# Kernel tuning notes

Measured on AMD Instinct MI355X. Metric: run time of the kernel, lower is better.

## Reference

```python
import jax, jax.numpy as jnp
import numpy as np

D = 1024
H = 16
HD = D // H
B = 2
T = 2048


def setup_inputs() -> dict:
    key = jax.random.key(0)
    ks = jax.random.split(key, 5)
    x = jax.random.normal(ks[0], (B, T, D), dtype=jnp.float32)
    # PyTorch SDPA bool-mask semantics: True = attend. Causal lower-triangular.
    attn_mask = jnp.tril(jnp.ones((T, T), dtype=bool))
    w_qkv = jax.random.normal(ks[1], (3 * D, D), dtype=jnp.float32) * (1.0 / np.sqrt(D))
    b_qkv = jax.random.normal(ks[2], (3 * D,), dtype=jnp.float32) * 0.02
    w_proj = jax.random.normal(ks[3], (D, D), dtype=jnp.float32) * (1.0 / np.sqrt(D))
    b_proj = jax.random.normal(ks[4], (D,), dtype=jnp.float32) * 0.02
    return {"x": x, "attn_mask": attn_mask, "w_qkv": w_qkv, "b_qkv": b_qkv,
            "w_proj": w_proj, "b_proj": b_proj}


def reference(x, attn_mask, w_qkv, b_qkv, w_proj, b_proj):
    b, t, d = x.shape
    # fused QKV projection (torch Linear: y = x @ W.T + b)
    qkv = jnp.einsum('btd,ed->bte', x, w_qkv) + b_qkv  # [B,T,3D]
    q, k, v = jnp.split(qkv, 3, axis=-1)
    # [B,T,D] -> [B,H,T,hd]
    def heads(z):
        return z.reshape(b, t, H, HD).transpose(0, 2, 1, 3)
    q, k, v = heads(q), heads(k), heads(v)
    scale = 1.0 / jnp.sqrt(jnp.asarray(HD, dtype=x.dtype))
    scores = jnp.einsum('bhqd,bhkd->bhqk', q, k) * scale  # [B,H,T,T]
    neg_inf = jnp.asarray(jnp.finfo(x.dtype).min, dtype=x.dtype)
    scores = jnp.where(attn_mask, scores, neg_inf)
    attn = jax.nn.softmax(scores, axis=-1)
    y = jnp.einsum('bhqk,bhkd->bhqd', attn, v)  # [B,H,T,hd]
    y = y.transpose(0, 2, 1, 3).reshape(b, t, d)
    y = jnp.einsum('btd,ed->bte', y, w_proj) + b_proj
    return y
```

## Files before the change

### kernel.cpp

```cpp
#include <hip/hip_runtime.h>
#include <hip/hip_bf16.h>
#include <math.h>

#define D_MODEL 1024
#define NHEAD   16
#define HDIM    64
#define BATCH   2
#define SEQ     2048
#define MTOT    (BATCH * SEQ)

typedef unsigned short u16;
typedef short short8 __attribute__((ext_vector_type(8)));
typedef short short4v __attribute__((ext_vector_type(4)));
typedef float floatx4 __attribute__((ext_vector_type(4)));

#define LOG2E 1.44269504088896340736f

static __device__ __forceinline__ u16 f2b(float f) {
  union { __hip_bfloat16 h; u16 u; } cv;
  cv.h = __float2bfloat16(f);
  return cv.u;
}

typedef const __attribute__((address_space(1))) unsigned int guint;
typedef __attribute__((address_space(3))) unsigned int luint;
static __device__ __forceinline__ void gl_lds16(const u16* g, u16* l) {
  __builtin_amdgcn_global_load_lds((guint*)g, (luint*)l, 16, 0, 0);
}

__global__ __launch_bounds__(256) void cast3_f2b(
    const float* __restrict__ a, u16* __restrict__ ao, int na,
    const float* __restrict__ b, u16* __restrict__ bo, int nb,
    const float* __restrict__ c, u16* __restrict__ co) {
  int i = (blockIdx.x * 256 + threadIdx.x) * 4;
  const float* src;
  u16* dst;
  if (i < na) {
    src = a + i;
    dst = ao + i;
  } else if (i < na + nb) {
    src = b + (i - na);
    dst = bo + (i - na);
  } else {
    src = c + (i - na - nb);
    dst = co + (i - na - nb);
  }
  float4 v = *(const float4*)src;
  ushort4 o;
  o.x = f2b(v.x);
  o.y = f2b(v.y);
  o.z = f2b(v.z);
  o.w = f2b(v.w);
  *(ushort4*)dst = o;
}

template <int MODE>
__global__ __launch_bounds__(256) void gemm_bt_bf16(
    const u16* __restrict__ A, const u16* __restrict__ Bm,
    const float* __restrict__ bias, u16* __restrict__ Cq, u16* __restrict__ Ck,
    u16* __restrict__ Cvt, float* __restrict__ Cf, int M, int N, int K) {
  __shared__ u16 smem[17408];
  u16(*As)[128][32] = (u16(*)[128][32])smem;
  u16(*Bs)[128][32] = (u16(*)[128][32])(smem + 8192);

  const int tid = threadIdx.x;
  const int lane = tid & 63;
  const int wave = tid >> 6;
  const int wm = (wave >> 1) * 64;
  const int wn = (wave & 1) * 64;
  const int quad = lane >> 4;
  const int l15 = lane & 15;
  const int m0 = blockIdx.y * 128;
  const int n0 = blockIdx.x * 128;

  const int srow = wave * 16 + (lane >> 2);
  const int k8 = (lane & 3) * 8;

  const u16* gA0 = A + (size_t)(m0 + srow) * K + k8;
  const u16* gA1 = A + (size_t)(m0 + srow + 64) * K + k8;
  const u16* gB0 = Bm + (size_t)(n0 + srow) * K + k8;
  const u16* gB1 = Bm + (size_t)(n0 + srow + 64) * K + k8;

  floatx4 acc[4][4];
#pragma unroll
  for (int i = 0; i < 4; ++i)
#pragma unroll
    for (int j = 0; j < 4; ++j)
#pragma unroll
      for (int e = 0; e < 4; ++e) acc[i][j][e] = 0.0f;

  gl_lds16(gA0, &As[0][srow][k8]);
  gl_lds16(gA1, &As[0][srow + 64][k8]);
  gl_lds16(gB0, &Bs[0][srow][k8]);
  gl_lds16(gB1, &Bs[0][srow + 64][k8]);

  const int niter = K / 32;
  for (int kt = 0; kt < niter; ++kt) {
    const int cur = kt & 1;
    __syncthreads();
    if (kt + 1 < niter) {
      const int k0n = (kt + 1) * 32;
      gl_lds16(gA0 + k0n, &As[cur ^ 1][srow][k8]);
      gl_lds16(gA1 + k0n, &As[cur ^ 1][srow + 64][k8]);
      gl_lds16(gB0 + k0n, &Bs[cur ^ 1][srow][k8]);
      gl_lds16(gB1 + k0n, &Bs[cur ^ 1][srow + 64][k8]);
    }
    short8 af[4], bf[4];
#pragma unroll
    for (int i = 0; i < 4; ++i)
      af[i] = *(const short8*)&As[cur][wm + i * 16 + l15][quad * 8];
#pragma unroll
    for (int j = 0; j < 4; ++j)
      bf[j] = *(const short8*)&Bs[cur][wn + j * 16 + l15][quad * 8];
#pragma unroll
    for (int i = 0; i < 4; ++i)
#pragma unroll
      for (int j = 0; j < 4; ++j)
        acc[i][j] = __builtin_amdgcn_mfma_f32_16x16x32_bf16(af[i], bf[j],
                                                            acc[i][j], 0, 0, 0);
  }

  if (MODE == 0) {
    const int nbase = n0 + wn;
    const int sel = nbase >> 10;
    const int h = (nbase >> 6) & (NHEAD - 1);
    if (sel == 2) {
#pragma unroll
      for (int j = 0; j < 4; ++j) {
        const int n = nbase + j * 16 + l15;
        const float bv = bias[n];
        const int d = n & (HDIM - 1);
#pragma unroll
        for (int i = 0; i < 4; ++i) {
          const int mb = m0 + wm + i * 16 + quad * 4;
          const int b = mb >> 11;
          const int t = mb & (SEQ - 1);
          ushort4 o4;
          o4.x = f2b(acc[i][j][0] + bv);
          o4.y = f2b(acc[i][j][1] + bv);
          o4.z = f2b(acc[i][j][2] + bv);
          o4.w = f2b(acc[i][j][3] + bv);
          *(ushort4*)(Cvt + ((size_t)(b * NHEAD + h) * HDIM + d) * SEQ + t) = o4;
        }
      }
    } else {
      u16* dst = (sel == 0) ? Cq : Ck;
      __syncthreads();
      u16(*Ct)[68] = (u16(*)[68])(smem + wave * 4352);
#pragma unroll
      for (int j = 0; j < 4; ++j) {
        const float bv = bias[nbase + j * 16 + l15];
#pragma unroll
        for (int i = 0; i < 4; ++i)
#pragma unroll
          for (int r = 0; r < 4; ++r)
            Ct[i * 16 + quad * 4 + r][j * 16 + l15] = f2b(acc[i][j][r] + bv);
      }
      const int mb0 = m0 + wm;
      const int b = mb0 >> 11;
      const int t0 = mb0 & (SEQ - 1);
      u16* rowbase = dst + ((size_t)(b * NHEAD + h) * SEQ + t0) * HDIM;
      const int tr = lane >> 3;
      const int d8 = (lane & 7) * 8;
#pragma unroll
      for (int p = 0; p < 8; ++p) {
        const int row = p * 8 + tr;
        *(short8*)(rowbase + (size_t)row * HDIM + d8) =
            *(const short8*)&Ct[row][d8];
      }
    }
  } else {
#pragma unroll
    for (int j = 0; j < 4; ++j) {
      const int n = n0 + wn + j * 16 + l15;
      const float bv = bias[n];
#pragma unroll
      for (int i = 0; i < 4; ++i) {
        const int mb = m0 + wm + i * 16 + quad * 4;
#pragma unroll
        for (int r = 0; r < 4; ++r)
          Cf[(size_t)(mb + r) * N + n] = acc[i][j][r] + bv;
      }
    }
  }
}

__global__ __launch_bounds__(512) void flash_mfma(const u16* __restrict__ Qg,
                                                  const u16* __restrict__ Kg,
                                                  const u16* __restrict__ Vtg,
                                                  u16* __restrict__ Yb) {
  __shared__ u16 Qs[128][72];
  __shared__ u16 Ks[64][72];
  __shared__ u16 Vt[80][72];
  __shared__ u16 Pb[128][76];

  const int tid = threadIdx.x;
  const int lane = tid & 63;
  const int wave = tid >> 6;
  const int wrow = wave * 16;
  const int quad = lane >> 4;
  const int l15 = lane & 15;
  const int bh = blockIdx.y;
  const int b = bh >> 4;
  const int h = bh & (NHEAD - 1);

  const u16* Qp = Qg + (size_t)bh * SEQ * HDIM;
  const u16* Kp = Kg + (size_t)bh * SEQ * HDIM;
  const u16* Vp = Vtg + (size_t)bh * HDIM * SEQ;

  const int srow = tid >> 3;
  const int s8 = (tid & 7) * 8;

  const float scale2 = 0.125f * LOG2E;

  for (int idx = tid; idx < 16 * 36; idx += 512) {
    const int row = 64 + idx / 36;
    const int c2 = (idx % 36) * 2;
    *(unsigned int*)&Vt[row][c2] = (row == 64) ? 0x3F803F80u : 0u;
  }

#pragma unroll
  for (int phase = 0; phase < 2; ++phase) {
    const int qt = phase == 0 ? (8 + blockIdx.x) : (7 - blockIdx.x);
    const int q0 = qt * 128;

    __syncthreads();
#pragma unroll
    for (int l = 0; l < 2; ++l) {
      const int c = tid + l * 512;
      const int row = c >> 3;
      const int d0 = (c & 7) * 8;
      *(short8*)&Qs[row][d0] =
          *(const short8*)(Qp + (size_t)(q0 + row) * HDIM + d0);
    }

    floatx4 o[5];
#pragma unroll
    for (int c = 0; c < 5; ++c)
#pragma unroll
      for (int e = 0; e < 4; ++e) o[c][e] = 0.0f;

    const int nkt = 2 * qt + 2;
    short8 kv = *(const short8*)(Kp + (size_t)srow * HDIM + s8);
    short8 vv = *(const short8*)(Vp + (size_t)srow * SEQ + s8);

    for (int kt = 0; kt < nkt; ++kt) {
      const int k0 = kt * 64;
      __syncthreads();
      *(short8*)&Ks[srow][s8] = kv;
      *(short8*)&Vt[srow][s8] = vv;
      __syncthreads();
      if (kt + 1 < nkt) {
        kv = *(const short8*)(Kp + (size_t)(k0 + 64 + srow) * HDIM + s8);
        vv = *(const short8*)(Vp + (size_t)srow * SEQ + k0 + 64 + s8);
      }

      short8 aq[2], bk[4][2];
#pragma unroll
      for (int kk = 0; kk < 2; ++kk)
        aq[kk] = *(const short8*)&Qs[wrow + l15][kk * 32 + quad * 8];
#pragma unroll
      for (int c = 0; c < 4; ++c)
#pragma unroll
        for (int kk = 0; kk < 2; ++kk)
          bk[c][kk] = *(const short8*)&Ks[c * 16 + l15][kk * 32 + quad * 8];

      floatx4 s[4];
#pragma unroll
      for (int c = 0; c < 4; ++c) {
#pragma unroll
        for (int e = 0; e < 4; ++e) s[c][e] = 0.0f;
        s[c] = __builtin_amdgcn_mfma_f32_16x16x32_bf16(aq[0], bk[c][0], s[c],
                                                       0, 0, 0);
        s[c] = __builtin_amdgcn_mfma_f32_16x16x32_bf16(aq[1], bk[c][1], s[c],
                                                       0, 0, 0);
      }

      const bool msk = (k0 + 64 > q0);
      const int prow = wrow + quad * 4;
#pragma unroll
      for (int c = 0; c < 4; ++c)
#pragma unroll
        for (int r = 0; r < 4; ++r) {
          float v = s[c][r] * scale2;
          if (msk) {
            const int row = q0 + prow + r;
            const int col = k0 + c * 16 + l15;
            if (col > row) v = -INFINITY;
          }
          Pb[prow + r][c * 16 + l15] = f2b(exp2f(v));
        }

      short8 ap[2];
#pragma unroll
      for (int kk = 0; kk < 2; ++kk) {
        short4v lo = *(const short4v*)&Pb[wrow + l15][kk * 32 + quad * 8];
        short4v hi = *(const short4v*)&Pb[wrow + l15][kk * 32 + quad * 8 + 4];
        ap[kk][0] = lo[0];
        ap[kk][1] = lo[1];
        ap[kk][2] = lo[2];
        ap[kk][3] = lo[3];
        ap[kk][4] = hi[0];
        ap[kk][5] = hi[1];
        ap[kk][6] = hi[2];
        ap[kk][7] = hi[3];
      }
#pragma unroll
      for (int c = 0; c < 5; ++c) {
        short8 bv0 = *(const short8*)&Vt[c * 16 + l15][quad * 8];
        short8 bv1 = *(const short8*)&Vt[c * 16 + l15][32 + quad * 8];
        o[c] = __builtin_amdgcn_mfma_f32_16x16x32_bf16(ap[0], bv0, o[c], 0, 0,
                                                       0);
        o[c] = __builtin_amdgcn_mfma_f32_16x16x32_bf16(ap[1], bv1, o[c], 0, 0,
                                                       0);
      }
    }

#pragma unroll
    for (int r = 0; r < 4; ++r) {
      const float lr = __shfl(o[4][r], lane & 48);
      const float inv = 1.0f / lr;
      const int t = q0 + wrow + quad * 4 + r;
#pragma unroll
      for (int c = 0; c < 4; ++c)
        Yb[((size_t)b * SEQ + t) * D_MODEL + h * HDIM + c * 16 + l15] =
            f2b(o[c][r] * inv);
    }
  }
}

extern "C" void kernel_launch(void* const* d_in, const int* in_sizes, int n_in,
                              void* d_out, int out_size, void* d_ws,
                              size_t ws_size, hipStream_t stream) {
  const float* x = (const float*)d_in[0];
  const float* w_qkv = (const float*)d_in[2];
  const float* b_qkv = (const float*)d_in[3];
  const float* w_proj = (const float*)d_in[4];
  const float* b_proj = (const float*)d_in[5];
  float* out = (float*)d_out;

  const size_t nx = (size_t)MTOT * D_MODEL;
  const size_t nwq = (size_t)3 * D_MODEL * D_MODEL;
  const size_t nwp = (size_t)D_MODEL * D_MODEL;
  const size_t nqkv = (size_t)BATCH * NHEAD * SEQ * HDIM;

  u16* xb = (u16*)d_ws;
  u16* wqb = xb + nx;
  u16* wpb = wqb + nwq;
  u16* qb = wpb + nwp;
  u16* kb = qb + nqkv;
  u16* vtb = kb + nqkv;
  u16* yb = vtb + nqkv;

  cast3_f2b<<<dim3((nx + nwq + nwp) / 1024), dim3(256), 0, stream>>>(
      x, xb, (int)nx, w_qkv, wqb, (int)nwq, w_proj, wpb);

  gemm_bt_bf16<0><<<dim3(24, 32), dim3(256), 0, stream>>>(
      xb, wqb, b_qkv, qb, kb, vtb, nullptr, MTOT, 3 * D_MODEL, D_MODEL);
  flash_mfma<<<dim3(8, BATCH * NHEAD), dim3(512), 0, stream>>>(qb, kb, vtb,
                                                               yb);
  gemm_bt_bf16<1><<<dim3(8, 32), dim3(256), 0, stream>>>(
      yb, wpb, b_proj, nullptr, nullptr, nullptr, out, MTOT, D_MODEL, D_MODEL);
}
```

Before: 201.2 us.

## Rework flash attention with 32x32 MFMA, register P, and split-K waves

The attention kernel now uses 32x32x16 MFMA, computing S transposed (K·Q) so the bf16 probabilities stay in registers and go to the PV MFMA through a lane shuffle instead of an LDS round-trip. The row sum is accumulated in registers rather than through an appended ones-row in V. The eight waves split into four row groups times two key halves, with partial outputs reduced through LDS scratch at the end. Separately, the output projection GEMM is templated to use 64-row tiles, doubling block count to fill more CUs, at the cost of less B-tile reuse.

```diff
diff --git a/kernel.cpp b/kernel.cpp
--- a/kernel.cpp
+++ b/kernel.cpp
@@ -10,9 +10,10 @@
 #define MTOT    (BATCH * SEQ)
 
 typedef unsigned short u16;
+typedef unsigned int u32;
 typedef short short8 __attribute__((ext_vector_type(8)));
-typedef short short4v __attribute__((ext_vector_type(4)));
 typedef float floatx4 __attribute__((ext_vector_type(4)));
+typedef float floatx16 __attribute__((ext_vector_type(16)));
 
 #define LOG2E 1.44269504088896340736f
 
@@ -20,6 +21,11 @@
   union { __hip_bfloat16 h; u16 u; } cv;
   cv.h = __float2bfloat16(f);
   return cv.u;
+}
+static __device__ __forceinline__ float b2f(u16 u) {
+  union { float f; u32 i; } cv;
+  cv.i = ((u32)u) << 16;
+  return cv.f;
 }
 
 typedef const __attribute__((address_space(1))) unsigned int guint;
@@ -54,23 +60,26 @@
   *(ushort4*)dst = o;
 }
 
-template <int MODE>
+template <int MODE, int AR>
 __global__ __launch_bounds__(256) void gemm_bt_bf16(
     const u16* __restrict__ A, const u16* __restrict__ Bm,
     const float* __restrict__ bias, u16* __restrict__ Cq, u16* __restrict__ Ck,
     u16* __restrict__ Cvt, float* __restrict__ Cf, int M, int N, int K) {
-  __shared__ u16 smem[17408];
-  u16(*As)[128][32] = (u16(*)[128][32])smem;
-  u16(*Bs)[128][32] = (u16(*)[128][32])(smem + 8192);
+  constexpr int MI = AR / 32;
+  constexpr int SMREQ = 2 * (AR + 128) * 32;
+  constexpr int SM = (MODE == 0) ? (SMREQ > 17408 ? SMREQ : 17408) : SMREQ;
+  __shared__ u16 smem[SM];
+  u16(*As)[AR][32] = (u16(*)[AR][32])smem;
+  u16(*Bs)[128][32] = (u16(*)[128][32])(smem + 2 * AR * 32);
 
   const int tid = threadIdx.x;
   const int lane = tid & 63;
   const int wave = tid >> 6;
-  const int wm = (wave >> 1) * 64;
+  const int wm = (wave >> 1) * (AR / 2);
   const int wn = (wave & 1) * 64;
   const int quad = lane >> 4;
   const int l15 = lane & 15;
-  const int m0 = blockIdx.y * 128;
+  const int m0 = blockIdx.y * AR;
   const int n0 = blockIdx.x * 128;
 
   const int srow = wave * 16 + (lane >> 2);
@@ -81,16 +90,16 @@
   const u16* gB0 = Bm + (size_t)(n0 + srow) * K + k8;
   const u16* gB1 = Bm + (size_t)(n0 + srow + 64) * K + k8;
 
-  floatx4 acc[4][4];
-#pragma unroll
-  for (int i = 0; i < 4; ++i)
+  floatx4 acc[MI][4];
+#pragma unroll
+  for (int i = 0; i < MI; ++i)
 #pragma unroll
     for (int j = 0; j < 4; ++j)
 #pragma unroll
       for (int e = 0; e < 4; ++e) acc[i][j][e] = 0.0f;
 
   gl_lds16(gA0, &As[0][srow][k8]);
-  gl_lds16(gA1, &As[0][srow + 64][k8]);
+  if (AR == 128) gl_lds16(gA1, &As[0][srow + 64][k8]);
   gl_lds16(gB0, &Bs[0][srow][k8]);
   gl_lds16(gB1, &Bs[0][srow + 64][k8]);
 
@@ -101,19 +110,19 @@
     if (kt + 1 < niter) {
       const int k0n = (kt + 1) * 32;
       gl_lds16(gA0 + k0n, &As[cur ^ 1][srow][k8]);
-      gl_lds16(gA1 + k0n, &As[cur ^ 1][srow + 64][k8]);
+      if (AR == 128) gl_lds16(gA1 + k0n, &As[cur ^ 1][srow + 64][k8]);
       gl_lds16(gB0 + k0n, &Bs[cur ^ 1][srow][k8]);
       gl_lds16(gB1 + k0n, &Bs[cur ^ 1][srow + 64][k8]);
     }
-    short8 af[4], bf[4];
-#pragma unroll
-    for (int i = 0; i < 4; ++i)
+    short8 af[MI], bf[4];
+#pragma unroll
+    for (int i = 0; i < MI; ++i)
       af[i] = *(const short8*)&As[cur][wm + i * 16 + l15][quad * 8];
 #pragma unroll
     for (int j = 0; j < 4; ++j)
       bf[j] = *(const short8*)&Bs[cur][wn + j * 16 + l15][quad * 8];
 #pragma unroll
-    for (int i = 0; i < 4; ++i)
+    for (int i = 0; i < MI; ++i)
 #pragma unroll
       for (int j = 0; j < 4; ++j)
         acc[i][j] = __builtin_amdgcn_mfma_f32_16x16x32_bf16(af[i], bf[j],
@@ -131,7 +140,7 @@
         const float bv = bias[n];
         const int d = n & (HDIM - 1);
 #pragma unroll
-        for (int i = 0; i < 4; ++i) {
+        for (int i = 0; i < MI; ++i) {
           const int mb = m0 + wm + i * 16 + quad * 4;
           const int b = mb >> 11;
           const int t = mb & (SEQ - 1);
@@ -151,7 +160,7 @@
       for (int j = 0; j < 4; ++j) {
         const float bv = bias[nbase + j * 16 + l15];
 #pragma unroll
-        for (int i = 0; i < 4; ++i)
+        for (int i = 0; i < MI; ++i)
 #pragma unroll
           for (int r = 0; r < 4; ++r)
             Ct[i * 16 + quad * 4 + r][j * 16 + l15] = f2b(acc[i][j][r] + bv);
@@ -175,7 +184,7 @@
       const int n = n0 + wn + j * 16 + l15;
       const float bv = bias[n];
 #pragma unroll
-      for (int i = 0; i < 4; ++i) {
+      for (int i = 0; i < MI; ++i) {
         const int mb = m0 + wm + i * 16 + quad * 4;
 #pragma unroll
         for (int r = 0; r < 4; ++r)
@@ -189,17 +198,19 @@
                                                   const u16* __restrict__ Kg,
                                                   const u16* __restrict__ Vtg,
                                                   u16* __restrict__ Yb) {
-  __shared__ u16 Qs[128][72];
-  __shared__ u16 Ks[64][72];
-  __shared__ u16 Vt[80][72];
-  __shared__ u16 Pb[128][76];
+  __shared__ u16 pool[19456];
+  u16(*Qs)[76] = (u16(*)[76])pool;
+  u16(*Ks)[76] = (u16(*)[76])(pool + 9728);
+  u16(*Vt)[76] = (u16(*)[76])(pool + 14592);
+  float* scrO = (float*)pool;
 
   const int tid = threadIdx.x;
   const int lane = tid & 63;
   const int wave = tid >> 6;
-  const int wrow = wave * 16;
-  const int quad = lane >> 4;
-  const int l15 = lane & 15;
+  const int rg = wave & 3;
+  const int kh = wave >> 2;
+  const int l31 = lane & 31;
+  const int hh = lane >> 5;
   const int bh = blockIdx.y;
   const int b = bh >> 4;
   const int h = bh & (NHEAD - 1);
@@ -212,12 +223,6 @@
   const int s8 = (tid & 7) * 8;
 
   const float scale2 = 0.125f * LOG2E;
-
-  for (int idx = tid; idx < 16 * 36; idx += 512) {
-    const int row = 64 + idx / 36;
-    const int c2 = (idx % 36) * 2;
-    *(unsigned int*)&Vt[row][c2] = (row == 64) ? 0x3F803F80u : 0u;
-  }
 
 #pragma unroll
   for (int phase = 0; phase < 2; ++phase) {
@@ -234,11 +239,13 @@
           *(const short8*)(Qp + (size_t)(q0 + row) * HDIM + d0);
     }
 
-    floatx4 o[5];
-#pragma unroll
-    for (int c = 0; c < 5; ++c)
-#pragma unroll
-      for (int e = 0; e < 4; ++e) o[c][e] = 0.0f;
+    floatx16 o[2];
+#pragma unroll
+    for (int mb = 0; mb < 2; ++mb)
+#pragma unroll
+      for (int i = 0; i < 16; ++i) o[mb][i] = 0.0f;
+    float l_own = 0.0f;
+    short8 qf[4];
 
     const int nkt = 2 * qt + 2;
     short8 kv = *(const short8*)(Kp + (size_t)srow * HDIM + s8);
@@ -250,81 +257,97 @@
       *(short8*)&Ks[srow][s8] = kv;
       *(short8*)&Vt[srow][s8] = vv;
       __syncthreads();
+      if (kt == 0) {
+#pragma unroll
+        for (int ks = 0; ks < 4; ++ks)
+          qf[ks] = *(const short8*)&Qs[rg * 32 + l31][ks * 16 + hh * 8];
+      }
       if (kt + 1 < nkt) {
         kv = *(const short8*)(Kp + (size_t)(k0 + 64 + srow) * HDIM + s8);
         vv = *(const short8*)(Vp + (size_t)srow * SEQ + k0 + 64 + s8);
       }
 
-      short8 aq[2], bk[4][2];
-#pragma unroll
-      for (int kk = 0; kk < 2; ++kk)
-        aq[kk] = *(const short8*)&Qs[wrow + l15][kk * 32 + quad * 8];
-#pragma unroll
-      for (int c = 0; c < 4; ++c)
-#pragma unroll
-        for (int kk = 0; kk < 2; ++kk)
-          bk[c][kk] = *(const short8*)&Ks[c * 16 + l15][kk * 32 + quad * 8];
-
-      floatx4 s[4];
-#pragma unroll
-      for (int c = 0; c < 4; ++c) {
-#pragma unroll
-        for (int e = 0; e < 4; ++e) s[c][e] = 0.0f;
-        s[c] = __builtin_amdgcn_mfma_f32_16x16x32_bf16(aq[0], bk[c][0], s[c],
-                                                       0, 0, 0);
-        s[c] = __builtin_amdgcn_mfma_f32_16x16x32_bf16(aq[1], bk[c][1], s[c],
-                                                       0, 0, 0);
+      floatx16 st;
+#pragma unroll
+      for (int i = 0; i < 16; ++i) st[i] = 0.0f;
+#pragma unroll
+      for (int ks = 0; ks < 4; ++ks) {
+        short8 kf = *(const short8*)&Ks[kh * 32 + l31][ks * 16 + hh * 8];
+        st = __builtin_amdgcn_mfma_f32_32x32x16_bf16(kf, qf[ks], st, 0, 0, 0);
       }
 
       const bool msk = (k0 + 64 > q0);
-      const int prow = wrow + quad * 4;
-#pragma unroll
-      for (int c = 0; c < 4; ++c)
-#pragma unroll
-        for (int r = 0; r < 4; ++r) {
-          float v = s[c][r] * scale2;
-          if (msk) {
-            const int row = q0 + prow + r;
-            const int col = k0 + c * 16 + l15;
-            if (col > row) v = -INFINITY;
-          }
-          Pb[prow + r][c * 16 + l15] = f2b(exp2f(v));
+      const int rowg = q0 + rg * 32 + l31;
+      const int colb = k0 + kh * 32 + 4 * hh;
+      u32 pk[8];
+      float psum = 0.0f;
+#pragma unroll
+      for (int j = 0; j < 8; ++j) {
+        const int i0 = 2 * j;
+        float v0 = st[i0] * scale2;
+        float v1 = st[i0 + 1] * scale2;
+        if (msk) {
+          const int c0 = colb + (i0 & 3) + 8 * (i0 >> 2);
+          if (c0 > rowg) v0 = -INFINITY;
+          if (c0 + 1 > rowg) v1 = -INFINITY;
         }
-
-      short8 ap[2];
-#pragma unroll
-      for (int kk = 0; kk < 2; ++kk) {
-        short4v lo = *(const short4v*)&Pb[wrow + l15][kk * 32 + quad * 8];
-        short4v hi = *(const short4v*)&Pb[wrow + l15][kk * 32 + quad * 8 + 4];
-        ap[kk][0] = lo[0];
-        ap[kk][1] = lo[1];
-        ap[kk][2] = lo[2];
-        ap[kk][3] = lo[3];
-        ap[kk][4] = hi[0];
-        ap[kk][5] = hi[1];
-        ap[kk][6] = hi[2];
-        ap[kk][7] = hi[3];
-      }
-#pragma unroll
-      for (int c = 0; c < 5; ++c) {
-        short8 bv0 = *(const short8*)&Vt[c * 16 + l15][quad * 8];
-        short8 bv1 = *(const short8*)&Vt[c * 16 + l15][32 + quad * 8];
-        o[c] = __builtin_amdgcn_mfma_f32_16x16x32_bf16(ap[0], bv0, o[c], 0, 0,
-                                                       0);
-        o[c] = __builtin_amdgcn_mfma_f32_16x16x32_bf16(ap[1], bv1, o[c], 0, 0,
-                                                       0);
-      }
-    }
-
-#pragma unroll
-    for (int r = 0; r < 4; ++r) {
-      const float lr = __shfl(o[4][r], lane & 48);
-      const float inv = 1.0f / lr;
-      const int t = q0 + wrow + quad * 4 + r;
-#pragma unroll
-      for (int c = 0; c < 4; ++c)
-        Yb[((size_t)b * SEQ + t) * D_MODEL + h * HDIM + c * 16 + l15] =
-            f2b(o[c][r] * inv);
+        const u16 h0 = f2b(exp2f(v0));
+        const u16 h1 = f2b(exp2f(v1));
+        pk[j] = (u32)h0 | ((u32)h1 << 16);
+        psum += b2f(h0) + b2f(h1);
+      }
+      l_own += psum;
+      u32 qk[8];
+#pragma unroll
+      for (int j = 0; j < 8; ++j) qk[j] = __shfl_xor(pk[j], 32);
+
+#pragma unroll
+      for (int ks2 = 0; ks2 < 2; ++ks2) {
+        const int x = 4 * ks2;
+        u32 bu[4];
+        bu[0] = hh ? qk[x + 2] : pk[x + 0];
+        bu[1] = hh ? qk[x + 3] : pk[x + 1];
+        bu[2] = hh ? pk[x + 2] : qk[x + 0];
+        bu[3] = hh ? pk[x + 3] : qk[x + 1];
+        short8 pf = *(short8*)bu;
+#pragma unroll
+        for (int mb = 0; mb < 2; ++mb) {
+          short8 vf = *(const short8*)&Vt[mb * 32 + l31]
+                                        [kh * 32 + ks2 * 16 + hh * 8];
+          o[mb] =
+              __builtin_amdgcn_mfma_f32_32x32x16_bf16(vf, pf, o[mb], 0, 0, 0);
+        }
+      }
+    }
+
+    const float l_half = l_own + __shfl_xor(l_own, 32);
+    __syncthreads();
+    if (wave >= 4) {
+      float* base = scrO + (wave - 4) * 33 * 64;
+#pragma unroll
+      for (int mb = 0; mb < 2; ++mb)
+#pragma unroll
+        for (int i = 0; i < 16; ++i) base[(mb * 16 + i) * 64 + lane] = o[mb][i];
+      base[32 * 64 + lane] = l_half;
+    }
+    __syncthreads();
+    if (wave < 4) {
+      const float* base = scrO + wave * 33 * 64;
+      const float ltot = l_half + base[32 * 64 + lane];
+      const float inv = 1.0f / ltot;
+      const int t = q0 + rg * 32 + l31;
+      u16* yrow = Yb + ((size_t)b * SEQ + t) * D_MODEL + h * HDIM;
+#pragma unroll
+      for (int mb = 0; mb < 2; ++mb)
+#pragma unroll
+        for (int s = 0; s < 4; ++s) {
+          ushort4 o4;
+          o4.x = f2b((o[mb][4 * s + 0] + base[(mb * 16 + 4 * s + 0) * 64 + lane]) * inv);
+          o4.y = f2b((o[mb][4 * s + 1] + base[(mb * 16 + 4 * s + 1) * 64 + lane]) * inv);
+          o4.z = f2b((o[mb][4 * s + 2] + base[(mb * 16 + 4 * s + 2) * 64 + lane]) * inv);
+          o4.w = f2b((o[mb][4 * s + 3] + base[(mb * 16 + 4 * s + 3) * 64 + lane]) * inv);
+          *(ushort4*)(yrow + mb * 32 + 8 * s + 4 * hh) = o4;
+        }
     }
   }
 }
@@ -355,10 +378,10 @@
   cast3_f2b<<<dim3((nx + nwq + nwp) / 1024), dim3(256), 0, stream>>>(
       x, xb, (int)nx, w_qkv, wqb, (int)nwq, w_proj, wpb);
 
-  gemm_bt_bf16<0><<<dim3(24, 32), dim3(256), 0, stream>>>(
+  gemm_bt_bf16<0, 128><<<dim3(24, 32), dim3(256), 0, stream>>>(
       xb, wqb, b_qkv, qb, kb, vtb, nullptr, MTOT, 3 * D_MODEL, D_MODEL);
   flash_mfma<<<dim3(8, BATCH * NHEAD), dim3(512), 0, stream>>>(qb, kb, vtb,
                                                                yb);
-  gemm_bt_bf16<1><<<dim3(8, 32), dim3(256), 0, stream>>>(
+  gemm_bt_bf16<1, 64><<<dim3(8, 64), dim3(256), 0, stream>>>(
       yb, wpb, b_proj, nullptr, nullptr, nullptr, out, MTOT, D_MODEL, D_MODEL);
 }
```

Measured after the change: 236.0 us. +17.3%, slower.

## Shrink flash query tile to 64 rows and halve output-projection M tile

Applied to the files above, without the earlier changes.

The flash attention kernel now processes 64-row query tiles with 256 threads and twice as many blocks. Shared rows are padded to 76 so the P fragment loads as one 16-byte read. The output projection GEMM is templated on its M-tile and launched with 64-row tiles, doubling its grid. The goal is more blocks across the CUs and less causal-mask waste, at the cost of less K/V reuse per block and more loop overhead.

```diff
diff --git a/kernel.cpp b/kernel.cpp
--- a/kernel.cpp
+++ b/kernel.cpp
@@ -10,8 +10,8 @@
 #define MTOT    (BATCH * SEQ)
 
 typedef unsigned short u16;
+typedef unsigned int u32;
 typedef short short8 __attribute__((ext_vector_type(8)));
-typedef short short4v __attribute__((ext_vector_type(4)));
 typedef float floatx4 __attribute__((ext_vector_type(4)));
 
 #define LOG2E 1.44269504088896340736f
@@ -54,23 +54,26 @@
   *(ushort4*)dst = o;
 }
 
-template <int MODE>
+template <int MODE, int AR>
 __global__ __launch_bounds__(256) void gemm_bt_bf16(
     const u16* __restrict__ A, const u16* __restrict__ Bm,
     const float* __restrict__ bias, u16* __restrict__ Cq, u16* __restrict__ Ck,
     u16* __restrict__ Cvt, float* __restrict__ Cf, int M, int N, int K) {
-  __shared__ u16 smem[17408];
-  u16(*As)[128][32] = (u16(*)[128][32])smem;
-  u16(*Bs)[128][32] = (u16(*)[128][32])(smem + 8192);
+  constexpr int MI = AR / 32;
+  constexpr int SMREQ = 2 * (AR + 128) * 32;
+  constexpr int SM = (MODE == 0) ? (SMREQ > 17408 ? SMREQ : 17408) : SMREQ;
+  __shared__ u16 smem[SM];
+  u16(*As)[AR][32] = (u16(*)[AR][32])smem;
+  u16(*Bs)[128][32] = (u16(*)[128][32])(smem + 2 * AR * 32);
 
   const int tid = threadIdx.x;
   const int lane = tid & 63;
   const int wave = tid >> 6;
-  const int wm = (wave >> 1) * 64;
+  const int wm = (wave >> 1) * (AR / 2);
   const int wn = (wave & 1) * 64;
   const int quad = lane >> 4;
   const int l15 = lane & 15;
-  const int m0 = blockIdx.y * 128;
+  const int m0 = blockIdx.y * AR;
   const int n0 = blockIdx.x * 128;
 
   const int srow = wave * 16 + (lane >> 2);
@@ -81,16 +84,16 @@
   const u16* gB0 = Bm + (size_t)(n0 + srow) * K + k8;
   const u16* gB1 = Bm + (size_t)(n0 + srow + 64) * K + k8;
 
-  floatx4 acc[4][4];
-#pragma unroll
-  for (int i = 0; i < 4; ++i)
+  floatx4 acc[MI][4];
+#pragma unroll
+  for (int i = 0; i < MI; ++i)
 #pragma unroll
     for (int j = 0; j < 4; ++j)
 #pragma unroll
       for (int e = 0; e < 4; ++e) acc[i][j][e] = 0.0f;
 
   gl_lds16(gA0, &As[0][srow][k8]);
-  gl_lds16(gA1, &As[0][srow + 64][k8]);
+  if (AR == 128) gl_lds16(gA1, &As[0][srow + 64][k8]);
   gl_lds16(gB0, &Bs[0][srow][k8]);
   gl_lds16(gB1, &Bs[0][srow + 64][k8]);
 
@@ -101,19 +104,19 @@
     if (kt + 1 < niter) {
       const int k0n = (kt + 1) * 32;
       gl_lds16(gA0 + k0n, &As[cur ^ 1][srow][k8]);
-      gl_lds16(gA1 + k0n, &As[cur ^ 1][srow + 64][k8]);
+      if (AR == 128) gl_lds16(gA1 + k0n, &As[cur ^ 1][srow + 64][k8]);
       gl_lds16(gB0 + k0n, &Bs[cur ^ 1][srow][k8]);
       gl_lds16(gB1 + k0n, &Bs[cur ^ 1][srow + 64][k8]);
     }
-    short8 af[4], bf[4];
-#pragma unroll
-    for (int i = 0; i < 4; ++i)
+    short8 af[MI], bf[4];
+#pragma unroll
+    for (int i = 0; i < MI; ++i)
       af[i] = *(const short8*)&As[cur][wm + i * 16 + l15][quad * 8];
 #pragma unroll
     for (int j = 0; j < 4; ++j)
       bf[j] = *(const short8*)&Bs[cur][wn + j * 16 + l15][quad * 8];
 #pragma unroll
-    for (int i = 0; i < 4; ++i)
+    for (int i = 0; i < MI; ++i)
 #pragma unroll
       for (int j = 0; j < 4; ++j)
         acc[i][j] = __builtin_amdgcn_mfma_f32_16x16x32_bf16(af[i], bf[j],
@@ -131,7 +134,7 @@
         const float bv = bias[n];
         const int d = n & (HDIM - 1);
 #pragma unroll
-        for (int i = 0; i < 4; ++i) {
+        for (int i = 0; i < MI; ++i) {
           const int mb = m0 + wm + i * 16 + quad * 4;
           const int b = mb >> 11;
           const int t = mb & (SEQ - 1);
@@ -151,7 +154,7 @@
       for (int j = 0; j < 4; ++j) {
         const float bv = bias[nbase + j * 16 + l15];
 #pragma unroll
-        for (int i = 0; i < 4; ++i)
+        for (int i = 0; i < MI; ++i)
 #pragma unroll
           for (int r = 0; r < 4; ++r)
             Ct[i * 16 + quad * 4 + r][j * 16 + l15] = f2b(acc[i][j][r] + bv);
@@ -175,7 +178,7 @@
       const int n = n0 + wn + j * 16 + l15;
       const float bv = bias[n];
 #pragma unroll
-      for (int i = 0; i < 4; ++i) {
+      for (int i = 0; i < MI; ++i) {
         const int mb = m0 + wm + i * 16 + quad * 4;
 #pragma unroll
         for (int r = 0; r < 4; ++r)
@@ -185,14 +188,14 @@
   }
 }
 
-__global__ __launch_bounds__(512) void flash_mfma(const u16* __restrict__ Qg,
+__global__ __launch_bounds__(256) void flash_mfma(const u16* __restrict__ Qg,
                                                   const u16* __restrict__ Kg,
                                                   const u16* __restrict__ Vtg,
                                                   u16* __restrict__ Yb) {
-  __shared__ u16 Qs[128][72];
-  __shared__ u16 Ks[64][72];
-  __shared__ u16 Vt[80][72];
-  __shared__ u16 Pb[128][76];
+  __shared__ u16 Qs[64][76];
+  __shared__ u16 Ks[64][76];
+  __shared__ u16 Vt[80][76];
+  __shared__ u16 Pb[64][76];
 
   const int tid = threadIdx.x;
   const int lane = tid & 63;
@@ -208,30 +211,29 @@
   const u16* Kp = Kg + (size_t)bh * SEQ * HDIM;
   const u16* Vp = Vtg + (size_t)bh * HDIM * SEQ;
 
-  const int srow = tid >> 3;
-  const int s8 = (tid & 7) * 8;
+  const int srow = tid >> 2;
+  const int sc = (tid & 3) * 16;
 
   const float scale2 = 0.125f * LOG2E;
 
-  for (int idx = tid; idx < 16 * 36; idx += 512) {
-    const int row = 64 + idx / 36;
-    const int c2 = (idx % 36) * 2;
-    *(unsigned int*)&Vt[row][c2] = (row == 64) ? 0x3F803F80u : 0u;
+  for (int idx = tid; idx < 16 * 38; idx += 256) {
+    const int row = 64 + idx / 38;
+    const int c2 = (idx % 38) * 2;
+    *(u32*)&Vt[row][c2] = (row == 64 && c2 < 64) ? 0x3F803F80u : 0u;
   }
 
 #pragma unroll
   for (int phase = 0; phase < 2; ++phase) {
-    const int qt = phase == 0 ? (8 + blockIdx.x) : (7 - blockIdx.x);
-    const int q0 = qt * 128;
+    const int qt = phase == 0 ? (16 + blockIdx.x) : (15 - blockIdx.x);
+    const int q0 = qt * 64;
 
     __syncthreads();
-#pragma unroll
-    for (int l = 0; l < 2; ++l) {
-      const int c = tid + l * 512;
-      const int row = c >> 3;
-      const int d0 = (c & 7) * 8;
-      *(short8*)&Qs[row][d0] =
-          *(const short8*)(Qp + (size_t)(q0 + row) * HDIM + d0);
+    {
+      const u16* qsrc = Qp + (size_t)(q0 + srow) * HDIM + sc;
+      short8 qv0 = *(const short8*)qsrc;
+      short8 qv1 = *(const short8*)(qsrc + 8);
+      *(short8*)&Qs[srow][sc] = qv0;
+      *(short8*)&Qs[srow][sc + 8] = qv1;
     }
 
     floatx4 o[5];
@@ -240,19 +242,27 @@
 #pragma unroll
       for (int e = 0; e < 4; ++e) o[c][e] = 0.0f;
 
-    const int nkt = 2 * qt + 2;
-    short8 kv = *(const short8*)(Kp + (size_t)srow * HDIM + s8);
-    short8 vv = *(const short8*)(Vp + (size_t)srow * SEQ + s8);
+    const int nkt = qt + 1;
+    short8 kv0 = *(const short8*)(Kp + (size_t)srow * HDIM + sc);
+    short8 kv1 = *(const short8*)(Kp + (size_t)srow * HDIM + sc + 8);
+    short8 vv0 = *(const short8*)(Vp + (size_t)srow * SEQ + sc);
+    short8 vv1 = *(const short8*)(Vp + (size_t)srow * SEQ + sc + 8);
 
     for (int kt = 0; kt < nkt; ++kt) {
       const int k0 = kt * 64;
       __syncthreads();
-      *(short8*)&Ks[srow][s8] = kv;
-      *(short8*)&Vt[srow][s8] = vv;
+      *(short8*)&Ks[srow][sc] = kv0;
+      *(short8*)&Ks[srow][sc + 8] = kv1;
+      *(short8*)&Vt[srow][sc] = vv0;
+      *(short8*)&Vt[srow][sc + 8] = vv1;
       __syncthreads();
       if (kt + 1 < nkt) {
-        kv = *(const short8*)(Kp + (size_t)(k0 + 64 + srow) * HDIM + s8);
-        vv = *(const short8*)(Vp + (size_t)srow * SEQ + k0 + 64 + s8);
+        const u16* kp = Kp + (size_t)(k0 + 64 + srow) * HDIM + sc;
+        const u16* vp = Vp + (size_t)srow * SEQ + k0 + 64 + sc;
+        kv0 = *(const short8*)kp;
+        kv1 = *(const short8*)(kp + 8);
+        vv0 = *(const short8*)vp;
+        vv1 = *(const short8*)(vp + 8);
       }
 
       short8 aq[2], bk[4][2];
@@ -276,7 +286,7 @@
                                                        0, 0, 0);
       }
 
-      const bool msk = (k0 + 64 > q0);
+      const bool msk = (kt == nkt - 1);
       const int prow = wrow + quad * 4;
 #pragma unroll
       for (int c = 0; c < 4; ++c)
@@ -293,18 +303,8 @@
 
       short8 ap[2];
 #pragma unroll
-      for (int kk = 0; kk < 2; ++kk) {
-        short4v lo = *(const short4v*)&Pb[wrow + l15][kk * 32 + quad * 8];
-        short4v hi = *(const short4v*)&Pb[wrow + l15][kk * 32 + quad * 8 + 4];
-        ap[kk][0] = lo[0];
-        ap[kk][1] = lo[1];
-        ap[kk][2] = lo[2];
-        ap[kk][3] = lo[3];
-        ap[kk][4] = hi[0];
-        ap[kk][5] = hi[1];
-        ap[kk][6] = hi[2];
-        ap[kk][7] = hi[3];
-      }
+      for (int kk = 0; kk < 2; ++kk)
+        ap[kk] = *(const short8*)&Pb[wrow + l15][kk * 32 + quad * 8];
 #pragma unroll
       for (int c = 0; c < 5; ++c) {
         short8 bv0 = *(const short8*)&Vt[c * 16 + l15][quad * 8];
@@ -355,10 +355,10 @@
   cast3_f2b<<<dim3((nx + nwq + nwp) / 1024), dim3(256), 0, stream>>>(
       x, xb, (int)nx, w_qkv, wqb, (int)nwq, w_proj, wpb);
 
-  gemm_bt_bf16<0><<<dim3(24, 32), dim3(256), 0, stream>>>(
+  gemm_bt_bf16<0, 128><<<dim3(24, 32), dim3(256), 0, stream>>>(
       xb, wqb, b_qkv, qb, kb, vtb, nullptr, MTOT, 3 * D_MODEL, D_MODEL);
-  flash_mfma<<<dim3(8, BATCH * NHEAD), dim3(512), 0, stream>>>(qb, kb, vtb,
-                                                               yb);
-  gemm_bt_bf16<1><<<dim3(8, 32), dim3(256), 0, stream>>>(
+  flash_mfma<<<dim3(16, BATCH * NHEAD), dim3(256), 0, stream>>>(qb, kb, vtb,
+                                                                yb);
+  gemm_bt_bf16<1, 64><<<dim3(8, 64), dim3(256), 0, stream>>>(
       yb, wpb, b_proj, nullptr, nullptr, nullptr, out, MTOT, D_MODEL, D_MODEL);
 }
```

After: 195.2 us. -3.0%, faster.
